# Optimization experiments

Measured on AMD Instinct MI355X. Metric: run time of the kernel, lower is better.

## Reference

```python
import jax, jax.numpy as jnp
import numpy as np

N = 100000
E = 3200000
F_IN = 256
HID = 128


def _dconv_k1(x_cat, w, b):
    # torch_geometric_temporal DConv with K=1:
    # H = X @ W[0,0] + X @ W[1,0] + b   (no graph propagation for K=1)
    return x_cat @ (w[0, 0] + w[1, 0]) + b


def _dcrnn_cell(x, h, wz, bz, wr, br, wh, bh):
    xh = jnp.concatenate([x, h], axis=1)
    z = jax.nn.sigmoid(_dconv_k1(xh, wz, bz))
    r = jax.nn.sigmoid(_dconv_k1(xh, wr, br))
    xrh = jnp.concatenate([x, r * h], axis=1)
    h_tilde = jnp.tanh(_dconv_k1(xrh, wh, bh))
    return z * h + (1.0 - z) * h_tilde


def setup_inputs() -> dict:
    key = jax.random.key(0)
    ks = jax.random.split(key, 16)

    def gw(k, shape):
        fan_in = shape[-2]
        return jax.random.normal(k, shape, dtype=jnp.float32) / np.sqrt(fan_in)

    inp = {
        "x": jax.random.normal(ks[0], (N, F_IN), dtype=jnp.float32),
        "edge_index": jax.random.randint(ks[1], (2, E), 0, N, dtype=jnp.int64 if jax.config.jax_enable_x64 else jnp.int32),
        "edge_weight": jax.random.uniform(ks[2], (E,), dtype=jnp.float32),
        "w_z1": gw(ks[3], (2, 1, F_IN + HID, HID)), "b_z1": jnp.zeros((HID,), jnp.float32),
        "w_r1": gw(ks[4], (2, 1, F_IN + HID, HID)), "b_r1": jnp.zeros((HID,), jnp.float32),
        "w_h1": gw(ks[5], (2, 1, F_IN + HID, HID)), "b_h1": jnp.zeros((HID,), jnp.float32),
        "w_z2": gw(ks[6], (2, 1, HID + HID // 2, HID // 2)), "b_z2": jnp.zeros((HID // 2,), jnp.float32),
        "w_r2": gw(ks[7], (2, 1, HID + HID // 2, HID // 2)), "b_r2": jnp.zeros((HID // 2,), jnp.float32),
        "w_h2": gw(ks[8], (2, 1, HID + HID // 2, HID // 2)), "b_h2": jnp.zeros((HID // 2,), jnp.float32),
        "w_lin1": gw(ks[9], (HID // 2, 16)), "b_lin1": jnp.zeros((16,), jnp.float32),
        "w_lin2": gw(ks[10], (16, 1)), "b_lin2": jnp.zeros((1,), jnp.float32),
    }
    return inp


def reference(x, edge_index, edge_weight,
              w_z1, b_z1, w_r1, b_r1, w_h1, b_h1,
              w_z2, b_z2, w_r2, b_r2, w_h2, b_h2,
              w_lin1, b_lin1, w_lin2, b_lin2):
    # edge_index / edge_weight are unused in the K=1 DConv math (faithful to tgt source).
    h0 = jnp.zeros((x.shape[0], w_z1.shape[-1]), x.dtype)
    h = _dcrnn_cell(x, h0, w_z1, b_z1, w_r1, b_r1, w_h1, b_h1)
    h = jax.nn.relu(h)
    h0b = jnp.zeros((x.shape[0], w_z2.shape[-1]), x.dtype)
    h = _dcrnn_cell(h, h0b, w_z2, b_z2, w_r2, b_r2, w_h2, b_h2)
    h = jax.nn.relu(h)
    # Dropout(0.2) is identity at inference
    h = jax.nn.relu(h @ w_lin1 + b_lin1)
    return h @ w_lin2 + b_lin2
```

## Files before the change

### kernel.cpp

```cpp
#include <hip/hip_runtime.h>

typedef _Float16 f16;
typedef _Float16 f16x4 __attribute__((ext_vector_type(4)));
typedef _Float16 f16x8 __attribute__((ext_vector_type(8)));
typedef float    f32x4 __attribute__((ext_vector_type(4)));

#define N_ROWS 100000
#define RT 782
#define TPB 512
#define LSX 264
#define LSH1 136
#define LSH2 72

#define W1F_OFF 0
#define W1F_BYTES (256 * 256 * 2)
#define W2F_OFF W1F_BYTES

#define ARENA 67584
#define H1S 0
#define H2S 34816

__global__ void prep_w(const float* __restrict__ wz1, const float* __restrict__ wh1,
                       const float* __restrict__ wz2, const float* __restrict__ wh2,
                       f16* __restrict__ W1F, f16* __restrict__ W2F) {
    const int b = blockIdx.x, tid = threadIdx.x;
    if (b < 32) {
        int idx = b * 256 + tid;
        int l = idx & 63, itm = idx >> 6;
        int it = itm & 7, M = itm >> 3;
        int ln = l & 15, q = l >> 4;
        int col = M * 16 + ln;
        int k0 = it * 32 + q * 8;
        const float* w = (col < 128) ? wz1 : wh1;
        int cc = col & 127;
        f16x8 v;
#pragma unroll
        for (int j = 0; j < 8; ++j) {
            int k = k0 + j;
            v[j] = (f16)(w[k * 128 + cc] + w[384 * 128 + k * 128 + cc]);
        }
        *(f16x8*)&W1F[idx * 8] = v;
    } else {
        int idx = (b - 32) * 256 + tid;
        if (idx >= 2048) return;
        int l = idx & 63, tkc = idx >> 6;
        int kc = tkc & 3, t = tkc >> 2;
        int ln = l & 15, q = l >> 4;
        int col = (t < 4) ? (16 * t + ln) : (64 + 16 * (t - 4) + ln);
        int k0 = kc * 32 + q * 8;
        const float* w = (col < 64) ? wz2 : wh2;
        int cc = col & 63;
        f16x8 v;
#pragma unroll
        for (int j = 0; j < 8; ++j) {
            int k = k0 + j;
            v[j] = (f16)(w[k * 64 + cc] + w[192 * 64 + k * 64 + cc]);
        }
        *(f16x8*)&W2F[idx * 8] = v;
    }
}

__device__ __forceinline__ float gate(float zp, float hp) {
    float e2h = __expf(2.0f * fminf(hp, 15.0f));
    float ez  = __expf(zp);
    float r   = __builtin_amdgcn_rcpf((e2h + 1.0f) * (1.0f + ez));
    return fmaxf((e2h - 1.0f) * r, 0.0f);
}

__global__ __launch_bounds__(TPB, 4) void fused(
    const float* __restrict__ x,
    const f16* __restrict__ W1F, const f16* __restrict__ W2F,
    const float* __restrict__ bz1, const float* __restrict__ bh1,
    const float* __restrict__ bz2, const float* __restrict__ bh2,
    const float* __restrict__ wl1, const float* __restrict__ bl1,
    const float* __restrict__ wl2, const float* __restrict__ bl2,
    float* __restrict__ out)
{
    __shared__ __align__(16) char arena[ARENA];
    const int tid = threadIdx.x, lane = tid & 63, wave = tid >> 6;
    const int ln = lane & 15, quad = lane >> 4;
    const int r0 = blockIdx.x * 128;

    const int xr = tid >> 2, xcg = tid & 3;
    int gxr = r0 + xr; if (gxr >= N_ROWS) gxr = N_ROWS - 1;
    const float* xp = x + (size_t)gxr * 256 + (xcg << 3);

    f16* Xs = (f16*)arena;
#pragma unroll 2
    for (int kc = 0; kc < 8; ++kc) {
        f32x4 a = __builtin_nontemporal_load((const f32x4*)(xp + kc * 32));
        f32x4 b = __builtin_nontemporal_load((const f32x4*)(xp + kc * 32 + 4));
        *(f16x8*)&Xs[xr * LSX + kc * 32 + (xcg << 3)] =
            (f16x8){(f16)a[0],(f16)a[1],(f16)a[2],(f16)a[3],
                    (f16)b[0],(f16)b[1],(f16)b[2],(f16)b[3]};
    }

    const f16* wbz = W1F + ((size_t)(wave * 8) * 64 + lane) * 8;
    const f16* wbh = W1F + ((size_t)((wave + 8) * 8) * 64 + lane) * 8;

    __syncthreads();

    f32x4 acc[2][8];
#pragma unroll
    for (int a = 0; a < 2; ++a)
#pragma unroll
        for (int b = 0; b < 8; ++b) acc[a][b] = (f32x4){0.f, 0.f, 0.f, 0.f};

#pragma unroll
    for (int it = 0; it < 8; ++it) {
        f16x8 afz = *(const f16x8*)(wbz + it * 512);
        f16x8 afh = *(const f16x8*)(wbh + it * 512);
        f16x8 bf[8];
#pragma unroll
        for (int nt = 0; nt < 8; ++nt)
            bf[nt] = *(const f16x8*)&Xs[(16 * nt + ln) * LSX + it * 32 + quad * 8];
#pragma unroll
        for (int nt = 0; nt < 8; ++nt)
            acc[0][nt] = __builtin_amdgcn_mfma_f32_16x16x32_f16(afz, bf[nt], acc[0][nt], 0, 0, 0);
#pragma unroll
        for (int nt = 0; nt < 8; ++nt)
            acc[1][nt] = __builtin_amdgcn_mfma_f32_16x16x32_f16(afh, bf[nt], acc[1][nt], 0, 0, 0);
    }
    __syncthreads();

    const int c = wave & 3, rh = wave >> 2;
    f16x8 w2f[2][4];
#pragma unroll
    for (int kc = 0; kc < 4; ++kc) {
        w2f[0][kc] = *(const f16x8*)(W2F + ((size_t)((c    ) * 4 + kc) * 64 + lane) * 8);
        w2f[1][kc] = *(const f16x8*)(W2F + ((size_t)((c + 4) * 4 + kc) * 64 + lane) * 8);
    }

    f16* h1s = (f16*)(arena + H1S);
    {
        const int jg0 = 16 * wave + (quad << 2);
        const float4 zb = *(const float4*)(bz1 + jg0);
        const float4 hb = *(const float4*)(bh1 + jg0);
#pragma unroll
        for (int nt = 0; nt < 8; ++nt) {
            const int row = 16 * nt + ln;
            f16x4 pk;
#pragma unroll
            for (int i = 0; i < 4; ++i)
                pk[i] = (f16)gate(acc[0][nt][i] + (&zb.x)[i],
                                  acc[1][nt][i] + (&hb.x)[i]);
            *(f16x4*)&h1s[row * LSH1 + jg0] = pk;
        }
    }
    __syncthreads();

    f32x4 acc2[2][4];
#pragma unroll
    for (int a = 0; a < 2; ++a)
#pragma unroll
        for (int b = 0; b < 4; ++b) acc2[a][b] = (f32x4){0.f, 0.f, 0.f, 0.f};
#pragma unroll
    for (int kc = 0; kc < 4; ++kc) {
        f16x8 bf[4];
#pragma unroll
        for (int nt = 0; nt < 4; ++nt)
            bf[nt] = *(const f16x8*)&h1s[(16 * (4 * rh + nt) + ln) * LSH1 + kc * 32 + quad * 8];
#pragma unroll
        for (int m = 0; m < 2; ++m)
#pragma unroll
            for (int nt = 0; nt < 4; ++nt)
                acc2[m][nt] = __builtin_amdgcn_mfma_f32_16x16x32_f16(w2f[m][kc], bf[nt], acc2[m][nt], 0, 0, 0);
    }

    f16* h2s = (f16*)(arena + H2S);
    {
        const int jg0 = 16 * c + (quad << 2);
        const float4 zb = *(const float4*)(bz2 + jg0);
        const float4 hb = *(const float4*)(bh2 + jg0);
#pragma unroll
        for (int nt = 0; nt < 4; ++nt) {
            const int row = 16 * (4 * rh + nt) + ln;
            f16x4 pk;
#pragma unroll
            for (int i = 0; i < 4; ++i)
                pk[i] = (f16)gate(acc2[0][nt][i] + (&zb.x)[i],
                                  acc2[1][nt][i] + (&hb.x)[i]);
            *(f16x4*)&h2s[row * LSH2 + jg0] = pk;
        }
    }
    __syncthreads();

    const float blv = bl1[ln], wlv = wl2[ln], bl2v = bl2[0];
    f16x8 bfr[2];
#pragma unroll
    for (int kc = 0; kc < 2; ++kc)
#pragma unroll
        for (int j = 0; j < 8; ++j)
            bfr[kc][j] = (f16)wl1[(32 * kc + 8 * quad + j) * 16 + ln];

    f32x4 acc3 = (f32x4){0.f, 0.f, 0.f, 0.f};
#pragma unroll
    for (int kc = 0; kc < 2; ++kc) {
        f16x8 af = *(const f16x8*)&h2s[(16 * wave + ln) * LSH2 + kc * 32 + quad * 8];
        acc3 = __builtin_amdgcn_mfma_f32_16x16x32_f16(af, bfr[kc], acc3, 0, 0, 0);
    }
#pragma unroll
    for (int i = 0; i < 4; ++i) {
        float v = fmaxf(acc3[i] + blv, 0.0f) * wlv;
        v += __shfl_xor(v, 1);
        v += __shfl_xor(v, 2);
        v += __shfl_xor(v, 4);
        v += __shfl_xor(v, 8);
        if (ln == 0) {
            const int row = r0 + 16 * wave + (quad << 2) + i;
            if (row < N_ROWS) out[row] = v + bl2v;
        }
    }
}

extern "C" void kernel_launch(void* const* d_in, const int* in_sizes, int n_in,
                              void* d_out, int out_size, void* d_ws, size_t ws_size,
                              hipStream_t stream) {
    const float* x   = (const float*)d_in[0];
    const float* wz1 = (const float*)d_in[3];
    const float* bz1 = (const float*)d_in[4];
    const float* wh1 = (const float*)d_in[7];
    const float* bh1 = (const float*)d_in[8];
    const float* wz2 = (const float*)d_in[9];
    const float* bz2 = (const float*)d_in[10];
    const float* wh2 = (const float*)d_in[13];
    const float* bh2 = (const float*)d_in[14];
    const float* wl1 = (const float*)d_in[15];
    const float* bl1 = (const float*)d_in[16];
    const float* wl2 = (const float*)d_in[17];
    const float* bl2 = (const float*)d_in[18];

    char* ws = (char*)d_ws;
    f16* W1F = (f16*)(ws + W1F_OFF);
    f16* W2F = (f16*)(ws + W2F_OFF);
    float* out = (float*)d_out;

    prep_w<<<40, 256, 0, stream>>>(wz1, wh1, wz2, wh2, W1F, W2F);
    fused<<<RT, TPB, 0, stream>>>(x, W1F, W2F, bz1, bh1, bz2, bh2,
                                  wl1, bl1, wl2, bl2, out);
}
```

Measured before the change: 221.4 us.

## Software-pipeline x loads with per-chunk MFMA in the first GEMM

Instead of staging the whole 256-wide x tile into LDS before computing, the kernel now loads one 32-column chunk at a time. It converts and stores that chunk to LDS, syncs, issues the next chunk's global and weight loads, then runs that chunk's MFMAs. The aim is to hide global load latency behind matrix math. The cost is eight block-wide barriers per tile and fewer outstanding global loads per thread at any moment, which may reduce memory-level parallelism.

After: 219.2 us. About the same (-1.0%).

```diff
diff --git a/kernel.cpp b/kernel.cpp
--- a/kernel.cpp
+++ b/kernel.cpp
@@ -86,40 +86,42 @@
     const float* xp = x + (size_t)gxr * 256 + (xcg << 3);
 
     f16* Xs = (f16*)arena;
-#pragma unroll 2
-    for (int kc = 0; kc < 8; ++kc) {
-        f32x4 a = __builtin_nontemporal_load((const f32x4*)(xp + kc * 32));
-        f32x4 b = __builtin_nontemporal_load((const f32x4*)(xp + kc * 32 + 4));
-        *(f16x8*)&Xs[xr * LSX + kc * 32 + (xcg << 3)] =
-            (f16x8){(f16)a[0],(f16)a[1],(f16)a[2],(f16)a[3],
-                    (f16)b[0],(f16)b[1],(f16)b[2],(f16)b[3]};
-    }
 
     const f16* wbz = W1F + ((size_t)(wave * 8) * 64 + lane) * 8;
     const f16* wbh = W1F + ((size_t)((wave + 8) * 8) * 64 + lane) * 8;
 
-    __syncthreads();
-
     f32x4 acc[2][8];
 #pragma unroll
     for (int a = 0; a < 2; ++a)
 #pragma unroll
         for (int b = 0; b < 8; ++b) acc[a][b] = (f32x4){0.f, 0.f, 0.f, 0.f};
 
-#pragma unroll
-    for (int it = 0; it < 8; ++it) {
-        f16x8 afz = *(const f16x8*)(wbz + it * 512);
-        f16x8 afh = *(const f16x8*)(wbh + it * 512);
-        f16x8 bf[8];
-#pragma unroll
-        for (int nt = 0; nt < 8; ++nt)
-            bf[nt] = *(const f16x8*)&Xs[(16 * nt + ln) * LSX + it * 32 + quad * 8];
-#pragma unroll
-        for (int nt = 0; nt < 8; ++nt)
-            acc[0][nt] = __builtin_amdgcn_mfma_f32_16x16x32_f16(afz, bf[nt], acc[0][nt], 0, 0, 0);
-#pragma unroll
-        for (int nt = 0; nt < 8; ++nt)
-            acc[1][nt] = __builtin_amdgcn_mfma_f32_16x16x32_f16(afh, bf[nt], acc[1][nt], 0, 0, 0);
+    f32x4 pa = __builtin_nontemporal_load((const f32x4*)(xp));
+    f32x4 pb = __builtin_nontemporal_load((const f32x4*)(xp + 4));
+    f16x8 afz = *(const f16x8*)(wbz);
+    f16x8 afh = *(const f16x8*)(wbh);
+
+#pragma unroll
+    for (int s = 0; s < 8; ++s) {
+        *(f16x8*)&Xs[xr * LSX + s * 32 + (xcg << 3)] =
+            (f16x8){(f16)pa[0],(f16)pa[1],(f16)pa[2],(f16)pa[3],
+                    (f16)pb[0],(f16)pb[1],(f16)pb[2],(f16)pb[3]};
+        __syncthreads();
+        f16x8 afz_n, afh_n;
+        if (s < 7) {
+            pa = __builtin_nontemporal_load((const f32x4*)(xp + (s + 1) * 32));
+            pb = __builtin_nontemporal_load((const f32x4*)(xp + (s + 1) * 32 + 4));
+            afz_n = *(const f16x8*)(wbz + (s + 1) * 512);
+            afh_n = *(const f16x8*)(wbh + (s + 1) * 512);
+        }
+        __builtin_amdgcn_sched_barrier(0);
+#pragma unroll
+        for (int nt = 0; nt < 8; ++nt) {
+            f16x8 bf = *(const f16x8*)&Xs[(16 * nt + ln) * LSX + s * 32 + quad * 8];
+            acc[0][nt] = __builtin_amdgcn_mfma_f32_16x16x32_f16(afz, bf, acc[0][nt], 0, 0, 0);
+            acc[1][nt] = __builtin_amdgcn_mfma_f32_16x16x32_f16(afh, bf, acc[1][nt], 0, 0, 0);
+        }
+        afz = afz_n; afh = afh_n;
     }
     __syncthreads();
 
```
